# Optimization experiments

Measured on AMD Instinct MI355X. Metric: run time of the kernel, lower is better.

## Reference

```python
import jax, jax.numpy as jnp
import numpy as np

N = 50000   # nodes
E = 800000  # edges (avg degree 16)
C = 64      # in_channels == out_channels


def _linear_params(key, fan_in, fan_out):
    kw, kb = jax.random.split(key)
    s = 1.0 / np.sqrt(fan_in)
    W = jax.random.uniform(kw, (fan_out, fan_in), minval=-s, maxval=s, dtype=jnp.float32)
    b = jax.random.uniform(kb, (fan_out,), minval=-s, maxval=s, dtype=jnp.float32)
    return W, b


def setup_inputs() -> dict:
    key = jax.random.key(0)
    ks = jax.random.split(key, 12)
    scalar = jax.random.normal(ks[0], (N, C), dtype=jnp.float32)
    vector = jax.random.normal(ks[1], (N, 3, C), dtype=jnp.float32)
    position = jax.random.normal(ks[2], (N, 3), dtype=jnp.float32)
    edge_index = jax.random.randint(ks[3], (2, E), 0, N, dtype=jnp.int64)
    edge_attr = jax.random.uniform(ks[4], (E,), dtype=jnp.float32)
    # Scalar_Conv params
    Wss, bss = _linear_params(ks[5], 2 * C, C)   # s_to_s
    Wvs, bvs = _linear_params(ks[6], 2 * C, C)   # v_to_s
    Wsl, bsl = _linear_params(ks[7], 2 * C, C)   # scalar_linear
    # Vector_Conv params
    Wsv, bsv = _linear_params(ks[8], 2 * C, C)   # s_to_v
    Wvv, bvv = _linear_params(ks[9], 2 * C, C)   # v_to_v
    Wvl, bvl = _linear_params(ks[10], 2 * C, C)  # vector_linear
    return dict(scalar=scalar, vector=vector, position=position,
                edge_index=edge_index, edge_attr=edge_attr,
                Wss=Wss, bss=bss, Wvs=Wvs, bvs=bvs, Wsl=Wsl, bsl=bsl,
                Wsv=Wsv, bsv=bsv, Wvv=Wvv, bvv=bvv, Wvl=Wvl, bvl=bvl)


def _norm(edge_index, edge_attr, num_nodes):
    # B=True path: edge_attr-weighted symmetric degree normalization
    row, col = edge_index[0], edge_index[1]
    deg = jax.ops.segment_sum(edge_attr, col, num_segments=num_nodes)
    deg_safe = jnp.where(deg > 0, deg, 1.0)
    dis = jnp.where(deg > 0, deg_safe ** -0.5, 0.0)
    return row, col, dis[row] * dis[col] * edge_attr


def _forward(scalar, vector, position, edge_index, edge_attr,
             Wss, bss, Wvs, bvs, Wsl, bsl, Wsv, bsv, Wvv, bvv, Wvl, bvl):
    num_nodes = scalar.shape[0]
    row, col = _norm(edge_index, edge_attr, num_nodes)[:2]
    _, _, norm = _norm(edge_index, edge_attr, num_nodes)
    # PyG: _i = target (col), _j = source (row); aggregate at col
    s_i, s_j = scalar[col], scalar[row]            # [E,C]
    v_i, v_j = vector[col], vector[row]            # [E,3,C]
    pos = position[col] - position[row]            # [E,3]
    s_cat = jnp.concatenate([s_i, s_j], axis=-1)   # [E,2C]
    v_cat = jnp.concatenate([v_i, v_j], axis=-1)   # [E,3,2C]

    # ---- Scalar_Conv messages ----
    s2s = jax.nn.silu(s_cat @ Wss.T + bss)                          # [E,C]
    v2s = v_cat @ Wvs.T + bvs                                       # [E,3,C]
    v2s = jax.nn.silu(jnp.sum(v2s * pos[:, :, None], axis=1))       # [E,C]
    s_msg = (jnp.concatenate([s2s, v2s], axis=-1) @ Wsl.T + bsl)    # [E,C]
    s_msg = norm[:, None] * s_msg
    s_agg = jax.ops.segment_sum(s_msg, col, num_segments=num_nodes)

    # ---- Vector_Conv messages ----
    s2v = s_cat @ Wsv.T + bsv                                       # [E,C]
    s2v = jnp.tanh(s2v[:, None, :] * pos[:, :, None])               # [E,3,C]
    v2v = v_cat @ Wvv.T + bvv                                       # [E,3,C]
    v_msg = jnp.concatenate([v2v, s2v], axis=-1) @ Wvl.T + bvl      # [E,3,C]
    v_msg = norm[:, None, None] * v_msg
    v_agg = jax.ops.segment_sum(v_msg, col, num_segments=num_nodes)

    scalar_out = jax.nn.silu(s_agg) + scalar
    vector_out = jnp.tanh(v_agg) + vector
    return scalar_out, vector_out


def reference(scalar, vector, position, edge_index, edge_attr,
              Wss, bss, Wvs, bvs, Wsl, bsl, Wsv, bsv, Wvv, bvv, Wvl, bvl):
    return _forward(scalar, vector, position, edge_index, edge_attr,
                    Wss, bss, Wvs, bvs, Wsl, bsl, Wsv, bsv, Wvv, bvv, Wvl, bvl)
```

## Files before the change

### kernel.cpp

```cpp
#include <hip/hip_runtime.h>
#include <cstdint>
#include <cstddef>

typedef unsigned int   u32;
typedef unsigned short u16;
typedef __attribute__((ext_vector_type(8))) short bf16x8;
typedef __attribute__((ext_vector_type(4))) float f32x4;

__device__ __forceinline__ float bf2f(u32 bits16) { return __uint_as_float(bits16 << 16); }
__device__ __forceinline__ u16 f2bf(float f) {
  u32 u = __float_as_uint(f);
  u = u + 0x7FFFu + ((u >> 16) & 1u);
  return (u16)(u >> 16);
}
__device__ __forceinline__ u32 pk(float a, float b) {
  return (u32)f2bf(a) | ((u32)f2bf(b) << 16);
}
__device__ __forceinline__ float lo16(u32 w) { return bf2f(w & 0xFFFFu); }
__device__ __forceinline__ float hi16(u32 w) { return bf2f(w >> 16); }
__device__ __forceinline__ float frcp(float x) { return __builtin_amdgcn_rcpf(x); }
__device__ __forceinline__ float fexp2(float x) { return __builtin_amdgcn_exp2f(x); }

#define NL2E   (-1.4426950408889634f)
#define TWOL2E (2.8853900817779268f)
#define CNTSC  1073741824.0

__device__ __forceinline__ int load_idx(const int* eidx, int is64, long long pos) {
  if (is64) return (int)(((const long long*)eidx)[pos]);
  return eidx[pos];
}

__global__ void k_prep1(const float* Wvl, const float* Wvv,
                        const float* bvv, const float* bvl,
                        const int* eidx, int E, int* flag,
                        float* WcTmp, float* bc) {
  int b = blockIdx.x, tid = threadIdx.x;
  if (b < 32) {
    int c = 2 * b + (tid >> 7), kk = tid & 127;
    float s = 0.f;
    for (int m = 0; m < 64; ++m) s += Wvl[c * 128 + m] * Wvv[m * 128 + kk];
    WcTmp[c * 128 + kk] = s;
  } else if (b == 32) {
    __shared__ int zc;
    if (tid == 0) zc = 0;
    __syncthreads();
    int n = (E < 1024) ? E : 1024;
    int local = 0;
    for (int i = tid; i < n; i += 256) {
      if (eidx[2 * i + 1] == 0) local++;
    }
    atomicAdd(&zc, local);
    __syncthreads();
    if (tid == 0) *flag = (zc >= (n >> 1)) ? 1 : 0;
  } else if (b == 33) {
    if (tid < 64) {
      float s = 0.f;
      for (int m = 0; m < 64; ++m) s += Wvl[tid * 128 + m] * bvv[m];
      bc[tid] = s + bvl[tid];
    }
  }
}

__global__ void k_prep2(const float* Wss, const float* Wsv, const float* Wvs,
                        const float* Wsl, const float* Wvl, const float* WcTmp,
                        u32* Wsl2, u32* Wpk, u16* Wtg) {
  int b = blockIdx.x, tid = threadIdx.x;
  if (b < 2) {
    for (int i = 0; i < 8; ++i) {
      int o = b * 2048 + i * 256 + tid;
      int h = o & 1, c = (o >> 1) & 63, g = o >> 7;
      int k = 4 * g + 2 * h;
      Wsl2[o] = pk(Wsl[c * 128 + k], Wsl[c * 128 + k + 1]);
    }
  } else if (b == 2) {
    for (int i = 0; i < 8; ++i) {
      int o = i * 256 + tid;
      int h = o & 1, c = (o >> 1) & 63, g = o >> 7;
      int k = 4 * g + 2 * h;
      Wpk[o] = pk(Wvl[c * 128 + 64 + k], Wvl[c * 128 + 64 + k + 1]);
    }
  } else {
    for (int i = 0; i < 16; ++i) {
      int p = (b - 3) * 4096 + i * 256 + tid;
      int r = p >> 6, k = p & 63;
      int g = (r >> 6) & 3, ch = r & 63;
      int src = ch * 128 + ((g & 2) ? 64 : 0) + k;
      float w;
      if (r < 256) w = (g & 1) ? Wsv[src] : Wss[src];
      else         w = (g & 1) ? WcTmp[src] : Wvs[src];
      u16 h = f2bf(w);
      Wtg[r * 128 + k] = h;
      Wtg[r * 128 + 64 + k] = f2bf(w - bf2f(h));
    }
  }
}

__global__ void k_deg(const int* eidx, const int* flag, const float* attr,
                      double* dpk, int E) {
  int e = blockIdx.x * 256 + threadIdx.x;
  if (e >= E) return;
  int is64 = *flag;
  int col = load_idx(eidx, is64, (long long)E + e);
  atomicAdd(&dpk[col], (double)attr[e] + CNTSC);
}

__global__ void k_scan_red(const double* dpk, int* blocksum, float* dis, int N) {
  __shared__ int lds[256];
  int tid = threadIdx.x, idx = blockIdx.x * 256 + tid;
  int c = 0;
  if (idx < N) {
    double p = dpk[idx];
    c = (int)(p * (1.0 / CNTSC));
    float dg = (float)(p - (double)c * CNTSC);
    dis[idx] = (dg > 0.f) ? rsqrtf(dg) : 0.f;
  }
  lds[tid] = c;
  __syncthreads();
  for (int off = 128; off > 0; off >>= 1) {
    if (tid < off) lds[tid] += lds[tid + off];
    __syncthreads();
  }
  if (tid == 0) blocksum[blockIdx.x] = lds[0];
}

__global__ void k_scan_mid(const int* blocksum, int* blockoff, int NB, int* rowptr, int N, int E) {
  __shared__ int lds[1024];
  int tid = threadIdx.x;
  int v = (tid < NB) ? blocksum[tid] : 0;
  lds[tid] = v;
  __syncthreads();
  for (int off = 1; off < 1024; off <<= 1) {
    int t = (tid >= off) ? lds[tid - off] : 0;
    __syncthreads();
    lds[tid] += t;
    __syncthreads();
  }
  if (tid < NB) blockoff[tid] = lds[tid] - v;
  if (tid == 0) rowptr[N] = E;
}

__global__ void k_scan_out(const double* dpk, const int* blockoff, int* rowptr, int* cursor, int N) {
  __shared__ int lds[256];
  int tid = threadIdx.x, idx = blockIdx.x * 256 + tid;
  int v = (idx < N) ? (int)(dpk[idx] * (1.0 / CNTSC)) : 0;
  lds[tid] = v;
  __syncthreads();
  for (int off = 1; off < 256; off <<= 1) {
    int t = (tid >= off) ? lds[tid - off] : 0;
    __syncthreads();
    lds[tid] += t;
    __syncthreads();
  }
  if (idx < N) {
    int o = blockoff[blockIdx.x] + lds[tid] - v;
    rowptr[idx] = o;
    cursor[idx] = o;
  }
}

__global__ void k_fill(const int* eidx, const int* flag, const float* attr, const float* dis,
                       const float* pos, int* cursor, float4* erecA, int* erecI, int E) {
  int e = blockIdx.x * 256 + threadIdx.x;
  if (e >= E) return;
  int is64 = *flag;
  int r  = load_idx(eidx, is64, e);
  int cl = load_idx(eidx, is64, (long long)E + e);
  float wr = dis[r] * attr[e];
  float dx = pos[cl * 3 + 0] - pos[r * 3 + 0];
  float dy = pos[cl * 3 + 1] - pos[r * 3 + 1];
  float dz = pos[cl * 3 + 2] - pos[r * 3 + 2];
  int p = atomicAdd(&cursor[cl], 1);
  erecA[p] = make_float4(wr, dx, dy, dz);
  erecI[p] = r;
}

__global__ __launch_bounds__(512, 4) void k_gemm_rec(
    const float* __restrict__ scalar, const float* __restrict__ vector,
    const u16* __restrict__ Wtg,
    uint4* __restrict__ rec_i4, uint4* __restrict__ rec_j4, int N) {
  __shared__ u32 smem[8192];
  u16*   Ax = (u16*)smem;
  float* Ep = (float*)smem;
  int tid = threadIdx.x, lane = tid & 63, wv = tid >> 6;
  int nb = blockIdx.x * 32;

  {
    int srow = tid >> 2, skq = tid & 3;
    const float* sp;
    int snode;
    if (srow < 32) { snode = nb + srow; sp = scalar + (size_t)snode * 64 + skq * 16; }
    else {
      int d = (srow - 32) >> 5, nl2 = (srow - 32) & 31;
      snode = nb + nl2;
      sp = vector + (size_t)snode * 192 + d * 64 + skq * 16;
    }
    bool valid = snode < N;
    u16 hi[16], lo[16];
    #pragma unroll
    for (int q = 0; q < 4; ++q) {
      float4 v = valid ? *(const float4*)(sp + 4 * q) : make_float4(0.f, 0.f, 0.f, 0.f);
      float xs[4] = {v.x, v.y, v.z, v.w};
      #pragma unroll
      for (int j = 0; j < 4; ++j) {
        u16 h = f2bf(xs[j]);
        hi[4 * q + j] = h;
        lo[4 * q + j] = f2bf(xs[j] - bf2f(h));
      }
    }
    int rs = srow & 7;
    #pragma unroll
    for (int c = 0; c < 2; ++c) {
      int lc = 2 * skq + c;
      uint4 wh, wl;
      wh.x = (u32)hi[8*c+0] | ((u32)hi[8*c+1] << 16);
      wh.y = (u32)hi[8*c+2] | ((u32)hi[8*c+3] << 16);
      wh.z = (u32)hi[8*c+4] | ((u32)hi[8*c+5] << 16);
      wh.w = (u32)hi[8*c+6] | ((u32)hi[8*c+7] << 16);
      wl.x = (u32)lo[8*c+0] | ((u32)lo[8*c+1] << 16);
      wl.y = (u32)lo[8*c+2] | ((u32)lo[8*c+3] << 16);
      wl.z = (u32)lo[8*c+4] | ((u32)lo[8*c+5] << 16);
      wl.w = (u32)lo[8*c+6] | ((u32)lo[8*c+7] << 16);
      *(uint4*)(Ax + srow * 128 + (lc ^ rs) * 8)        = wh;
      *(uint4*)(Ax + srow * 128 + ((8 + lc) ^ rs) * 8)  = wl;
    }
  }
  __syncthreads();

  int c0 = wv * 32;
  int bl = lane & 15, bh = lane >> 4;
  f32x4 acc[8][2];
  #pragma unroll
  for (int mt = 0; mt < 8; ++mt)
    #pragma unroll
    for (int nt = 0; nt < 2; ++nt)
      acc[mt][nt] = (f32x4){0.f, 0.f, 0.f, 0.f};

  #pragma unroll
  for (int kh = 0; kh < 2; ++kh) {
    int k0 = kh * 32;
    bf16x8 Bh[2][2], Bl[2][2];
    #pragma unroll
    for (int rg = 0; rg < 2; ++rg)
      #pragma unroll
      for (int nt = 0; nt < 2; ++nt) {
        size_t rr = (size_t)(rg * 256 + c0 + nt * 16 + bl) * 128 + k0 + bh * 8;
        Bh[rg][nt] = *(const bf16x8*)(Wtg + rr);
        Bl[rg][nt] = *(const bf16x8*)(Wtg + rr + 64);
      }
    #pragma unroll
    for (int mt = 0; mt < 8; ++mt) {
      int row = mt * 16 + bl;
      int ch = (k0 >> 3) + bh, rs = row & 7;
      bf16x8 Ah = *(const bf16x8*)(Ax + row * 128 + (ch ^ rs) * 8);
      bf16x8 Al = *(const bf16x8*)(Ax + row * 128 + ((8 + ch) ^ rs) * 8);
      int rg = (mt < 2) ? 0 : 1;
      #pragma unroll
      for (int nt = 0; nt < 2; ++nt) {
        f32x4 a = acc[mt][nt];
        a = __builtin_amdgcn_mfma_f32_16x16x32_bf16(Ah, Bh[rg][nt], a, 0, 0, 0);
        a = __builtin_amdgcn_mfma_f32_16x16x32_bf16(Al, Bh[rg][nt], a, 0, 0, 0);
        a = __builtin_amdgcn_mfma_f32_16x16x32_bf16(Ah, Bl[rg][nt], a, 0, 0, 0);
        acc[mt][nt] = a;
      }
    }
  }

  int ech = tid & 63, eng = tid >> 6;
  uint4 oi[4], oj[4];
  #pragma unroll
  for (int pg = 0; pg < 4; ++pg) {
    __syncthreads();
    #pragma unroll
    for (int mm = 0; mm < 2; ++mm) {
      int mt = 2 * pg + mm;
      #pragma unroll
      for (int nt = 0; nt < 2; ++nt)
        #pragma unroll
        for (int r = 0; r < 4; ++r) {
          int rl = mm * 16 + bh * 4 + r;
          Ep[rl * 256 + c0 + nt * 16 + bl] = acc[mt][nt][r];
        }
    }
    __syncthreads();
    #pragma unroll
    for (int q = 0; q < 4; ++q) {
      int nl2 = eng + 8 * q;
      float vi0 = Ep[nl2 * 256 + ech];
      float vi1 = Ep[nl2 * 256 + 64 + ech];
      float vj0 = Ep[nl2 * 256 + 128 + ech];
      float vj1 = Ep[nl2 * 256 + 192 + ech];
      if (pg == 0) {
        oi[q].x = pk(vi0, vi1);                  oj[q].x = pk(vj0, vj1);
      } else if (pg == 1) {
        oi[q].y = (u32)f2bf(vi0);                oj[q].y = (u32)f2bf(vj0);
        oi[q].z = (u32)f2bf(vi1) << 16;          oj[q].z = (u32)f2bf(vj1) << 16;
      } else if (pg == 2) {
        oi[q].y |= (u32)f2bf(vi0) << 16;         oj[q].y |= (u32)f2bf(vj0) << 16;
        oi[q].w = (u32)f2bf(vi1);                oj[q].w = (u32)f2bf(vj1);
      } else {
        oi[q].z |= (u32)f2bf(vi0);               oj[q].z |= (u32)f2bf(vj0);
        oi[q].w |= (u32)f2bf(vi1) << 16;         oj[q].w |= (u32)f2bf(vj1) << 16;
      }
    }
  }
  #pragma unroll
  for (int q = 0; q < 4; ++q) {
    int node = nb + eng + 8 * q;
    if (node < N) {
      rec_i4[(size_t)node * 64 + ech] = oi[q];
      rec_j4[(size_t)node * 64 + ech] = oj[q];
    }
  }
}

__global__ __launch_bounds__(512) void k_edges(
    const u16* __restrict__ rec_i, const u16* __restrict__ rec_j,
    const float4* __restrict__ erecA, const int* __restrict__ erecI,
    const int* __restrict__ rowptr, const float* __restrict__ dis,
    const float* __restrict__ scalar, const float* __restrict__ vector,
    const float* __restrict__ bss, const float* __restrict__ bvs,
    const float* __restrict__ bsv, const float* __restrict__ bsl,
    const u32* __restrict__ Wsl2g, const u32* __restrict__ Wpkg,
    const float* __restrict__ bcg,
    float* __restrict__ out_s, float* __restrict__ out_v, int N) {
  __shared__ u32 sWsl[4096];
  __shared__ u32 sWv[2048];
  __shared__ float sStage[8 * 128];
  int tid = threadIdx.x, lane = tid & 63, wv = tid >> 6;
  for (int o = tid; o < 4096; o += 512) sWsl[o] = Wsl2g[o];
  for (int o = tid; o < 2048; o += 512) sWv[o] = Wpkg[o];
  __syncthreads();

  int node = __builtin_amdgcn_readfirstlane((int)(blockIdx.x * 8) + wv);
  if (node >= N) node = N - 1;

  uint4 riv = *(const uint4*)(rec_i + ((size_t)node << 9) + lane * 8);
  float aiB  = lo16(riv.x) + bss[lane];
  float KciB = TWOL2E * (hi16(riv.x) + bsv[lane]);
  float Bvs  = bvs[lane];
  float bib0 = lo16(riv.y) + Bvs;
  float bib1 = hi16(riv.y) + Bvs;
  float bib2 = lo16(riv.z) + Bvs;
  float Pi0  = hi16(riv.z), Pi1 = lo16(riv.w), Pi2 = hi16(riv.w);
  float bsl_c = bsl[lane], bc_c = bcg[lane];
  float disc = dis[node];

  float us = 0, uv = 0, t0 = 0, t1 = 0, t2 = 0, g0 = 0, g1 = 0, g2 = 0, wa = 0;
  int rp = rowptr[node], re = rowptr[node + 1];
  u32 lane16 = (u32)lane << 4;
  const char* rjb = (const char*)rec_j;

  u32 ra = (u32)erecI[rp];
  u32 rb = (u32)erecI[rp + 1];
  uint4 pre0 = *(const uint4*)(rjb + ((ra << 10) + lane16));
  uint4 pre1 = *(const uint4*)(rjb + ((rb << 10) + lane16));
  int p = rp;
  #define EDGE_MATH(CUR, EV)                                                  \
    {                                                                         \
      float nrm = EV.x, dx = EV.y, dy = EV.z, dz = EV.w;                      \
      float aj  = lo16(CUR.x), cj  = hi16(CUR.x);                             \
      float bj0 = lo16(CUR.y), bj1 = hi16(CUR.y), bj2 = lo16(CUR.z);          \
      float rj0 = hi16(CUR.z), rj1 = lo16(CUR.w), rj2 = hi16(CUR.w);          \
      float xs  = aiB + aj;                                                   \
      float s2s = xs * frcp(1.f + fexp2(xs * NL2E));                          \
      float yv  = (bib0 + bj0) * dx;                                          \
      yv = fmaf(bib1 + bj1, dy, yv);                                          \
      yv = fmaf(bib2 + bj2, dz, yv);                                          \
      float v2s = yv * frcp(1.f + fexp2(yv * NL2E));                          \
      float qh  = fmaf(TWOL2E, cj, KciB);                                     \
      float th0 = fmaf(-2.f, frcp(1.f + fexp2(qh * dx)), 1.f);                \
      float th1 = fmaf(-2.f, frcp(1.f + fexp2(qh * dy)), 1.f);                \
      float th2 = fmaf(-2.f, frcp(1.f + fexp2(qh * dz)), 1.f);                \
      us = fmaf(nrm, s2s, us); uv = fmaf(nrm, v2s, uv);                       \
      t0 = fmaf(nrm, th0, t0); t1 = fmaf(nrm, th1, t1); t2 = fmaf(nrm, th2, t2);\
      g0 = fmaf(nrm, rj0, g0); g1 = fmaf(nrm, rj1, g1); g2 = fmaf(nrm, rj2, g2);\
      wa += nrm;                                                              \
    }
  for (; p + 1 < re; p += 2) {
    uint4 cur0 = pre0, cur1 = pre1;
    u32 rn0 = (u32)erecI[p + 2];
    u32 rn1 = (u32)erecI[p + 3];
    pre0 = *(const uint4*)(rjb + ((rn0 << 10) + lane16));
    pre1 = *(const uint4*)(rjb + ((rn1 << 10) + lane16));
    float4 e0 = erecA[p];
    float4 e1 = erecA[p + 1];
    EDGE_MATH(cur0, e0)
    EDGE_MATH(cur1, e1)
  }
  if (p < re) {
    uint4 cur0 = pre0;
    float4 e0 = erecA[p];
    EDGE_MATH(cur0, e0)
  }
  #undef EDGE_MATH

  us *= disc; uv *= disc;
  t0 *= disc; t1 *= disc; t2 *= disc;
  g0 *= disc; g1 *= disc; g2 *= disc;
  wa *= disc;

  float* mys = &sStage[wv * 128];
  mys[lane] = us; mys[64 + lane] = uv;
  __threadfence_block();
  float acc = wa * bsl_c;
  #pragma unroll
  for (int g = 0; g < 32; ++g) {
    float4 u = *(const float4*)&mys[4 * g];
    uint2 w = *(const uint2*)&sWsl[(g * 64 + lane) * 2];
    acc = fmaf(u.x, lo16(w.x), acc);
    acc = fmaf(u.y, hi16(w.x), acc);
    acc = fmaf(u.z, lo16(w.y), acc);
    acc = fmaf(u.w, hi16(w.y), acc);
  }
  size_t so = ((size_t)node << 6) + lane;
  out_s[so] = acc * frcp(1.f + fexp2(acc * NL2E)) + scalar[so];

  float gg[3] = {g0, g1, g2}, tt[3] = {t0, t1, t2}, Pi[3] = {Pi0, Pi1, Pi2};
  #pragma unroll
  for (int d = 0; d < 3; ++d) {
    size_t vo = (((size_t)node * 3 + d) << 6) + lane;
    float vid = vector[vo];
    __threadfence_block();
    mys[lane] = tt[d];
    __threadfence_block();
    float a2 = fmaf(wa, bc_c + Pi[d], gg[d]);
    #pragma unroll
    for (int g = 0; g < 16; ++g) {
      float4 tu = *(const float4*)&mys[4 * g];
      uint2 w = *(const uint2*)&sWv[(g * 64 + lane) * 2];
      a2 = fmaf(tu.x, lo16(w.x), a2); a2 = fmaf(tu.y, hi16(w.x), a2);
      a2 = fmaf(tu.z, lo16(w.y), a2); a2 = fmaf(tu.w, hi16(w.y), a2);
    }
    float th = fmaf(-2.f, frcp(1.f + fexp2(TWOL2E * a2)), 1.f);
    out_v[vo] = th + vid;
  }
}

extern "C" void kernel_launch(void* const* d_in, const int* in_sizes, int n_in,
                              void* d_out, int out_size, void* d_ws, size_t ws_size,
                              hipStream_t stream) {
  const float* scalar   = (const float*)d_in[0];
  const float* vector   = (const float*)d_in[1];
  const float* position = (const float*)d_in[2];
  const int*   eidx     = (const int*)d_in[3];
  const float* attr     = (const float*)d_in[4];
  const float* Wss = (const float*)d_in[5];
  const float* bss = (const float*)d_in[6];
  const float* Wvs = (const float*)d_in[7];
  const float* bvs = (const float*)d_in[8];
  const float* Wsl = (const float*)d_in[9];
  const float* bsl = (const float*)d_in[10];
  const float* Wsv = (const float*)d_in[11];
  const float* bsv = (const float*)d_in[12];
  const float* Wvv = (const float*)d_in[13];
  const float* bvv = (const float*)d_in[14];
  const float* Wvl = (const float*)d_in[15];
  const float* bvl = (const float*)d_in[16];

  int N = in_sizes[0] / 64;
  int E = in_sizes[4];
  int NB = (N + 255) / 256;

  char* wsb = (char*)d_ws;
  size_t off = 0;
  auto alloc = [&](size_t bytes) -> char* {
    char* p = wsb + off;
    off += (bytes + 255) & ~(size_t)255;
    return p;
  };
  double* dpk    = (double*)alloc((size_t)N * 8);
  int*    rowptr = (int*)alloc((size_t)(N + 1) * 4);
  int*    cursor = (int*)alloc((size_t)N * 4);
  float*  dis    = (float*)alloc((size_t)N * 4);
  int*    blocksum = (int*)alloc((size_t)NB * 4);
  int*    blockoff = (int*)alloc((size_t)NB * 4);
  float4* erecA  = (float4*)alloc((size_t)E * 16);
  int*    erecI  = (int*)alloc((size_t)(E + 64) * 4);
  u16*    rec_i  = (u16*)alloc((size_t)N * 512 * 2);
  u16*    rec_j  = (u16*)alloc((size_t)N * 512 * 2);
  u16*    Wtg    = (u16*)alloc(512 * 128 * 2);
  u32*    Wsl2   = (u32*)alloc(4096 * 4);
  u32*    Wpk    = (u32*)alloc(2048 * 4);
  float*  WcTmp  = (float*)alloc(64 * 128 * 4);
  float*  bc     = (float*)alloc(64 * 4);
  int*    flag   = (int*)alloc(4);
  (void)ws_size; (void)n_in; (void)out_size;

  hipMemsetAsync(dpk, 0, (size_t)((char*)rowptr - (char*)dpk), stream);
  hipMemsetAsync(erecI + E, 0, 64 * 4, stream);

  k_prep1<<<34, 256, 0, stream>>>(Wvl, Wvv, bvv, bvl, eidx, E, flag, WcTmp, bc);
  k_prep2<<<11, 256, 0, stream>>>(Wss, Wsv, Wvs, Wsl, Wvl, WcTmp, Wsl2, Wpk, Wtg);
  k_deg<<<(E + 255) / 256, 256, 0, stream>>>(eidx, flag, attr, dpk, E);
  k_scan_red<<<NB, 256, 0, stream>>>(dpk, blocksum, dis, N);
  k_scan_mid<<<1, 1024, 0, stream>>>(blocksum, blockoff, NB, rowptr, N, E);
  k_scan_out<<<NB, 256, 0, stream>>>(dpk, blockoff, rowptr, cursor, N);
  k_fill<<<(E + 255) / 256, 256, 0, stream>>>(eidx, flag, attr, dis, position, cursor, erecA, erecI, E);
  k_gemm_rec<<<(N + 31) / 32, 512, 0, stream>>>(scalar, vector, Wtg,
                                                (uint4*)rec_i, (uint4*)rec_j, N);
  k_edges<<<(N + 7) / 8, 512, 0, stream>>>(rec_i, rec_j, erecA, erecI, rowptr, dis,
                                           scalar, vector, bss, bvs, bsv, bsl,
                                           Wsl2, Wpk, bc,
                                           (float*)d_out, (float*)d_out + (size_t)N * 64, N);
}
```

Baseline: 431.4 us.

## Fold memsets into prep kernel and fuse degree scatter into GEMM launch

```diff
diff --git a/kernel.cpp b/kernel.cpp
--- a/kernel.cpp
+++ b/kernel.cpp
@@ -33,7 +33,8 @@
 __global__ void k_prep1(const float* Wvl, const float* Wvv,
                         const float* bvv, const float* bvl,
                         const int* eidx, int E, int* flag,
-                        float* WcTmp, float* bc) {
+                        float* WcTmp, float* bc,
+                        double* dpk, int* erecI, int N) {
   int b = blockIdx.x, tid = threadIdx.x;
   if (b < 32) {
     int c = 2 * b + (tid >> 7), kk = tid & 127;
@@ -58,6 +59,11 @@
       for (int m = 0; m < 64; ++m) s += Wvl[tid * 128 + m] * bvv[m];
       bc[tid] = s + bvl[tid];
     }
+  } else if (b == 34) {
+    if (tid < 64) erecI[E + tid] = 0;
+  } else {
+    int idx = (b - 35) * 256 + tid;
+    if (idx < N) dpk[idx] = 0.0;
   }
 }
 
@@ -93,15 +99,6 @@
       Wtg[r * 128 + 64 + k] = f2bf(w - bf2f(h));
     }
   }
-}
-
-__global__ void k_deg(const int* eidx, const int* flag, const float* attr,
-                      double* dpk, int E) {
-  int e = blockIdx.x * 256 + threadIdx.x;
-  if (e >= E) return;
-  int is64 = *flag;
-  int col = load_idx(eidx, is64, (long long)E + e);
-  atomicAdd(&dpk[col], (double)attr[e] + CNTSC);
 }
 
 __global__ void k_scan_red(const double* dpk, int* blocksum, float* dis, int N) {
@@ -174,14 +171,26 @@
   erecI[p] = r;
 }
 
-__global__ __launch_bounds__(512, 4) void k_gemm_rec(
+__global__ __launch_bounds__(512, 4) void k_gemm_deg(
     const float* __restrict__ scalar, const float* __restrict__ vector,
     const u16* __restrict__ Wtg,
-    uint4* __restrict__ rec_i4, uint4* __restrict__ rec_j4, int N) {
+    uint4* __restrict__ rec_i4, uint4* __restrict__ rec_j4, int N, int GB,
+    const int* __restrict__ eidx, const int* __restrict__ flag,
+    const float* __restrict__ attr, double* __restrict__ dpk, int E) {
   __shared__ u32 smem[8192];
+  int tid = threadIdx.x;
+  if ((int)blockIdx.x >= GB) {
+    int e = ((int)blockIdx.x - GB) * 512 + tid;
+    if (e < E) {
+      int is64 = *flag;
+      int col = load_idx(eidx, is64, (long long)E + e);
+      atomicAdd(&dpk[col], (double)attr[e] + CNTSC);
+    }
+    return;
+  }
   u16*   Ax = (u16*)smem;
   float* Ep = (float*)smem;
-  int tid = threadIdx.x, lane = tid & 63, wv = tid >> 6;
+  int lane = tid & 63, wv = tid >> 6;
   int nb = blockIdx.x * 32;
 
   {
@@ -486,18 +495,19 @@
   int*    flag   = (int*)alloc(4);
   (void)ws_size; (void)n_in; (void)out_size;
 
-  hipMemsetAsync(dpk, 0, (size_t)((char*)rowptr - (char*)dpk), stream);
-  hipMemsetAsync(erecI + E, 0, 64 * 4, stream);
-
-  k_prep1<<<34, 256, 0, stream>>>(Wvl, Wvv, bvv, bvl, eidx, E, flag, WcTmp, bc);
+  int GB = (N + 31) / 32;
+  int DB = (E + 511) / 512;
+
+  k_prep1<<<35 + NB, 256, 0, stream>>>(Wvl, Wvv, bvv, bvl, eidx, E, flag,
+                                       WcTmp, bc, dpk, erecI, N);
   k_prep2<<<11, 256, 0, stream>>>(Wss, Wsv, Wvs, Wsl, Wvl, WcTmp, Wsl2, Wpk, Wtg);
-  k_deg<<<(E + 255) / 256, 256, 0, stream>>>(eidx, flag, attr, dpk, E);
+  k_gemm_deg<<<GB + DB, 512, 0, stream>>>(scalar, vector, Wtg,
+                                          (uint4*)rec_i, (uint4*)rec_j, N, GB,
+                                          eidx, flag, attr, dpk, E);
   k_scan_red<<<NB, 256, 0, stream>>>(dpk, blocksum, dis, N);
   k_scan_mid<<<1, 1024, 0, stream>>>(blocksum, blockoff, NB, rowptr, N, E);
   k_scan_out<<<NB, 256, 0, stream>>>(dpk, blockoff, rowptr, cursor, N);
   k_fill<<<(E + 255) / 256, 256, 0, stream>>>(eidx, flag, attr, dis, position, cursor, erecA, erecI, E);
-  k_gemm_rec<<<(N + 31) / 32, 512, 0, stream>>>(scalar, vector, Wtg,
-                                                (uint4*)rec_i, (uint4*)rec_j, N);
   k_edges<<<(N + 7) / 8, 512, 0, stream>>>(rec_i, rec_j, erecA, erecI, rowptr, dis,
                                            scalar, vector, bss, bvs, bsv, bsl,
                                            Wsl2, Wpk, bc,
```

Result: faster. 405.4 us (-6.0%).
